# Performance work log

Hardware: AMD Instinct MI355X
Metric: run time of the kernel (lower is better)

The kernel has to match this reference:

```python
import jax, jax.numpy as jnp
import numpy as np
from jax import lax

DN = ('NCHW', 'OIHW', 'NCHW')

def setup_inputs() -> dict:
    key = jax.random.key(0)
    ks = jax.random.split(key, 7)
    s = 0.05  # keep activations tame through 32 chained blocks
    return {
        'x':  jax.random.normal(ks[0], (16, 256, 64, 64), dtype=jnp.float32),
        'w1': jax.random.normal(ks[1], (32, 4, 256, 1, 1), dtype=jnp.float32) * s,
        'b1': jax.random.normal(ks[2], (32, 4), dtype=jnp.float32) * s,
        'w2': jax.random.normal(ks[3], (32, 4, 4, 3, 3), dtype=jnp.float32) * s,
        'b2': jax.random.normal(ks[4], (32, 4), dtype=jnp.float32) * s,
        'w3': jax.random.normal(ks[5], (32, 256, 4, 1, 1), dtype=jnp.float32) * s,
        'b3': jax.random.normal(ks[6], (32, 256), dtype=jnp.float32) * s,
    }

def _block(x, w1, c1, w2, c2, w3, c3):
    # 1x1 reduce -> relu -> 3x3 same -> relu -> 1x1 expand -> relu
    h = jax.nn.relu(lax.conv_general_dilated(x, w1, (1, 1), 'VALID', dimension_numbers=DN)
                    + c1[None, :, None, None])
    h = jax.nn.relu(lax.conv_general_dilated(h, w2, (1, 1), 'SAME', dimension_numbers=DN)
                    + c2[None, :, None, None])
    h = jax.nn.relu(lax.conv_general_dilated(h, w3, (1, 1), 'VALID', dimension_numbers=DN)
                    + c3[None, :, None, None])
    return h

def reference(x, w1, b1, w2, b2, w3, b3):
    def step(carry, ws):
        xc, acc = carry
        xc = _block(xc, *ws)
        return (xc, acc + xc), None
    init = (x, jnp.zeros_like(x))
    (_, acc), _ = lax.scan(step, init, (w1, b1, w2, b2, w3, b3))
    return acc  # sum of all 32 block outputs, [16,256,64,64]
```

## Files before the change

kernel.cpp:

```cpp
#include <hip/hip_runtime.h>


#define NN 16
#define HH 64
#define WW 64
#define CIN 256
#define CB 4
#define NBLK 32
#define PXT 32

__device__ __forceinline__ int pxs(int px) { return px ^ ((px >> 3) & 7); }

__global__ __launch_bounds__(256) void phaseA(
    const float* __restrict__ x, const float* __restrict__ w1,
    const float* __restrict__ b1, float* __restrict__ h1out) {
  __shared__ float4 w1s[CIN];
  __shared__ float4 part[4][WW];
  int tid = threadIdx.x;
  for (int i = tid; i < CIN * CB; i += 256) {
    int o = i >> 8, c = i & 255;
    ((float*)&w1s[c])[o] = w1[i];
  }
  __syncthreads();
  int y = blockIdx.x, n = blockIdx.y;
  int chunk = tid >> 6, px = tid & 63;
  int cbase = chunk * 64;
  const float* xp = x + ((n * CIN + cbase) * HH + y) * WW + px;
  float s0 = 0.f, s1 = 0.f, s2 = 0.f, s3 = 0.f;
#pragma unroll 8
  for (int i = 0; i < 64; ++i) {
    float xv = xp[i * HH * WW];
    float4 wv = w1s[cbase + i];
    s0 = fmaf(xv, wv.x, s0);
    s1 = fmaf(xv, wv.y, s1);
    s2 = fmaf(xv, wv.z, s2);
    s3 = fmaf(xv, wv.w, s3);
  }
  part[chunk][px] = make_float4(s0, s1, s2, s3);
  __syncthreads();
  int px2 = tid >> 2, o = tid & 3;
  float v = ((float*)&part[0][px2])[o] + ((float*)&part[1][px2])[o] +
            ((float*)&part[2][px2])[o] + ((float*)&part[3][px2])[o];
  v += b1[o];
  h1out[((n * HH + y) * WW + px2) * CB + o] = fmaxf(v, 0.f);
}

__global__ __launch_bounds__(256, 2) void phaseB(
    const float* __restrict__ h1in, float* __restrict__ h1out,
    float* __restrict__ h2out,
    const float* __restrict__ w2, const float* __restrict__ b2,
    const float* __restrict__ w3, const float* __restrict__ b3,
    const float* __restrict__ w1n, const float* __restrict__ b1n,
    int compute_next) {
  __shared__ float4 wpk[CIN][2];
  __shared__ float4 b3p[64];
  __shared__ float4 h2sb[128];
  __shared__ __align__(16) float4 uni[2048];
  float4 (*h1t)[18] = (float4(*)[18])uni;
  float4* comb = (float4*)uni;

  int tid = threadIdx.x;
  int tx = blockIdx.x, ty = blockIdx.y, n = blockIdx.z;
  int x0 = tx * 16, y0 = ty * 8;

  {
    int c = tid;
    wpk[c][0] = *(const float4*)&w3[c * 4];
    float4 wt;
    wt.x = w1n[c];
    wt.y = w1n[256 + c];
    wt.z = w1n[512 + c];
    wt.w = w1n[768 + c];
    wpk[c][1] = wt;
    if (tid < 64) b3p[tid] = *(const float4*)&b3[tid * 4];
  }
  if (tid < 180) {
    int cy = tid / 18, cx = tid % 18;
    int gy = y0 + cy - 1, gx = x0 + cx - 1;
    float4 v = make_float4(0.f, 0.f, 0.f, 0.f);
    if (gy >= 0 && gy < HH && gx >= 0 && gx < WW)
      v = *(const float4*)&h1in[((n * HH + gy) * WW + gx) * CB];
    h1t[cy][cx] = v;
  }
  __syncthreads();

  if (tid < 128) {
    int lx = tid & 15, ly = tid >> 4;
    float4 hacc = make_float4(b2[0], b2[1], b2[2], b2[3]);
#pragma unroll
    for (int p = 0; p < 9; ++p) {
      int dy = p / 3, dx = p % 3;
      float4 hv = h1t[ly + dy][lx + dx];
#pragma unroll
      for (int i = 0; i < 4; ++i) {
        float hvi = (i == 0) ? hv.x : (i == 1) ? hv.y : (i == 2) ? hv.z : hv.w;
        hacc.x = fmaf(hvi, w2[(0 * 4 + i) * 9 + p], hacc.x);
        hacc.y = fmaf(hvi, w2[(1 * 4 + i) * 9 + p], hacc.y);
        hacc.z = fmaf(hvi, w2[(2 * 4 + i) * 9 + p], hacc.z);
        hacc.w = fmaf(hvi, w2[(3 * 4 + i) * 9 + p], hacc.w);
      }
    }
    float4 h2 = make_float4(fmaxf(hacc.x, 0.f), fmaxf(hacc.y, 0.f),
                            fmaxf(hacc.z, 0.f), fmaxf(hacc.w, 0.f));
    int gy = y0 + ly, gx = x0 + lx;
    int pxg = (n * HH + gy) * WW + gx;
    *(float4*)&h2out[pxg * CB] = h2;
    h2sb[pxs(tid)] = h2;
  }
  __syncthreads();

  int pg = tid & 15, q = tid >> 4;
  float4 h2r[8];
#pragma unroll
  for (int j = 0; j < 8; ++j) h2r[j] = h2sb[pxs(pg * 8 + j)];

  float4 tp[8];
#pragma unroll
  for (int j = 0; j < 8; ++j) tp[j] = make_float4(0.f, 0.f, 0.f, 0.f);

#pragma unroll
  for (int i4 = 0; i4 < 4; ++i4) {
    float4 bv = b3p[q * 4 + i4];
#pragma unroll
    for (int s = 0; s < 4; ++s) {
      int c = q * 16 + i4 * 4 + s;
      float b = (s == 0) ? bv.x : (s == 1) ? bv.y : (s == 2) ? bv.z : bv.w;
      float4 w3v = wpk[c][0];
      float4 wnv = wpk[c][1];
#pragma unroll
      for (int j = 0; j < 8; ++j) {
        float u = fmaf(h2r[j].x, w3v.x, b);
        u = fmaf(h2r[j].y, w3v.y, u);
        u = fmaf(h2r[j].z, w3v.z, u);
        u = fmaf(h2r[j].w, w3v.w, u);
        float v = fmaxf(u, 0.f);
        tp[j].x = fmaf(v, wnv.x, tp[j].x);
        tp[j].y = fmaf(v, wnv.y, tp[j].y);
        tp[j].z = fmaf(v, wnv.z, tp[j].z);
        tp[j].w = fmaf(v, wnv.w, tp[j].w);
      }
    }
  }

#pragma unroll
  for (int j = 0; j < 8; ++j)
    comb[q * 128 + pxs(pg * 8 + j)] = tp[j];
  __syncthreads();

  if (compute_next && tid < 128) {
    int p = tid;
    float4 t = comb[pxs(p)];
#pragma unroll
    for (int qq = 1; qq < 16; ++qq) {
      float4 pv = comb[qq * 128 + pxs(p)];
      t.x += pv.x; t.y += pv.y; t.z += pv.z; t.w += pv.w;
    }
    float4 r = make_float4(fmaxf(t.x + b1n[0], 0.f), fmaxf(t.y + b1n[1], 0.f),
                           fmaxf(t.z + b1n[2], 0.f), fmaxf(t.w + b1n[3], 0.f));
    int gy = y0 + (p >> 4), gx = x0 + (p & 15);
    *(float4*)&h1out[((n * HH + gy) * WW + gx) * CB] = r;
  }
}

__global__ __launch_bounds__(256, 4) void phaseC(
    const float* __restrict__ h2buf, const float* __restrict__ w3g,
    const float* __restrict__ b3g, float* __restrict__ out) {
  __shared__ float4 h2s[2][PXT];
  __shared__ float tr[CIN][PXT + 1];
  int tid = threadIdx.x;
  int p0 = blockIdx.x * PXT;
  int n = blockIdx.y;
  float acc[PXT];
#pragma unroll
  for (int i = 0; i < PXT; ++i) acc[i] = 0.f;

  if (tid < PXT)
    h2s[0][tid] = *(const float4*)&h2buf[((0 * NN + n) * 4096 + p0 + tid) * 4];
  __syncthreads();

  for (int k = 0; k < NBLK; ++k) {
    float4 wv = *(const float4*)&w3g[(k * 256 + tid) * 4];
    float bv = b3g[k * 256 + tid];
    if (k + 1 < NBLK && tid < PXT)
      h2s[(k + 1) & 1][tid] =
          *(const float4*)&h2buf[(((k + 1) * NN + n) * 4096 + p0 + tid) * 4];
    const float4* hb = h2s[k & 1];
#pragma unroll
    for (int i = 0; i < PXT; ++i) {
      float4 h = hb[i];
      float u = fmaf(h.w, wv.w,
                fmaf(h.z, wv.z, fmaf(h.y, wv.y, fmaf(h.x, wv.x, bv))));
      acc[i] += fmaxf(u, 0.f);
    }
    __syncthreads();
  }

#pragma unroll
  for (int i = 0; i < PXT; ++i) tr[tid][i] = acc[i];
  __syncthreads();
  int xi = tid & 31, cb = tid >> 5;
#pragma unroll
  for (int j = 0; j < 32; ++j) {
    int c = cb + j * 8;
    out[(n * CIN + c) * (HH * WW) + p0 + xi] = tr[c][xi];
  }
}

extern "C" void kernel_launch(void* const* d_in, const int* in_sizes, int n_in,
                              void* d_out, int out_size, void* d_ws, size_t ws_size,
                              hipStream_t stream) {
  const float* x  = (const float*)d_in[0];
  const float* w1 = (const float*)d_in[1];
  const float* b1 = (const float*)d_in[2];
  const float* w2 = (const float*)d_in[3];
  const float* b2 = (const float*)d_in[4];
  const float* w3 = (const float*)d_in[5];
  const float* b3 = (const float*)d_in[6];
  float* out = (float*)d_out;
  float* ws = (float*)d_ws;

  const int STATE = NN * HH * WW * CB;
  float* h1a = ws;
  float* h1b = ws + STATE;
  float* h2  = ws + 2 * STATE;

  phaseA<<<dim3(HH, NN), 256, 0, stream>>>(x, w1, b1, h1a);
  for (int k = 0; k < NBLK; ++k) {
    const float* hin = (k & 1) ? h1b : h1a;
    float* hout = (k & 1) ? h1a : h1b;
    int kn = (k < NBLK - 1) ? k + 1 : NBLK - 1;
    phaseB<<<dim3(4, 8, NN), 256, 0, stream>>>(
        hin, hout, h2 + k * STATE,
        w2 + k * 144, b2 + k * CB, w3 + k * 1024, b3 + k * 256,
        w1 + kn * 1024, b1 + kn * CB, (k < NBLK - 1) ? 1 : 0);
  }
  phaseC<<<dim3((HH * WW) / PXT, NN), 256, 0, stream>>>(h2, w3, b3, out);
}
```

Before: 481.9 us.

## Shrink phaseB tiles to 8x8 and re-tile phaseC over channels and pixels

phaseB now works on 8x8 pixel tiles with twice as many blocks and a launch bound of 4 blocks per CU. Each of its 256 threads computes one output channel of the 3x3 conv, instead of only 128 threads doing all four. The last block returns early and skips the unused next-h1 work. phaseC is re-tiled so each thread owns 4 channels by 8 pixels, prefetches the next block's w3/b3 into registers, and writes its output through a smaller shared transpose in four chunks. The aim is more parallelism and occupancy and fewer redundant loads, at the cost of more halo overhead per tile in phaseB and extra syncs in phaseC's output stage.

Result: no change. 472.9 us (-1.9%).

```diff
diff --git a/kernel.cpp b/kernel.cpp
--- a/kernel.cpp
+++ b/kernel.cpp
@@ -9,7 +9,7 @@
 #define NBLK 32
 #define PXT 32
 
-__device__ __forceinline__ int pxs(int px) { return px ^ ((px >> 3) & 7); }
+__device__ __forceinline__ int swz64(int i) { return i ^ ((i >> 2) & 7); }
 
 __global__ __launch_bounds__(256) void phaseA(
     const float* __restrict__ x, const float* __restrict__ w1,
@@ -45,7 +45,7 @@
   h1out[((n * HH + y) * WW + px2) * CB + o] = fmaxf(v, 0.f);
 }
 
-__global__ __launch_bounds__(256, 2) void phaseB(
+__global__ __launch_bounds__(256, 4) void phaseB(
     const float* __restrict__ h1in, float* __restrict__ h1out,
     float* __restrict__ h2out,
     const float* __restrict__ w2, const float* __restrict__ b2,
@@ -54,14 +54,14 @@
     int compute_next) {
   __shared__ float4 wpk[CIN][2];
   __shared__ float4 b3p[64];
-  __shared__ float4 h2sb[128];
-  __shared__ __align__(16) float4 uni[2048];
-  float4 (*h1t)[18] = (float4(*)[18])uni;
+  __shared__ float4 h2sb[64];
+  __shared__ __align__(16) float4 uni[1024];
+  float4 (*h1t)[12] = (float4(*)[12])uni;
   float4* comb = (float4*)uni;
 
   int tid = threadIdx.x;
-  int tx = blockIdx.x, ty = blockIdx.y, n = blockIdx.z;
-  int x0 = tx * 16, y0 = ty * 8;
+  int x0 = blockIdx.x * 8, y0 = blockIdx.y * 8;
+  int n = blockIdx.z;
 
   {
     int c = tid;
@@ -74,8 +74,8 @@
     wpk[c][1] = wt;
     if (tid < 64) b3p[tid] = *(const float4*)&b3[tid * 4];
   }
-  if (tid < 180) {
-    int cy = tid / 18, cx = tid % 18;
+  if (tid < 100) {
+    int cy = tid / 10, cx = tid % 10;
     int gy = y0 + cy - 1, gx = x0 + cx - 1;
     float4 v = make_float4(0.f, 0.f, 0.f, 0.f);
     if (gy >= 0 && gy < HH && gx >= 0 && gx < WW)
@@ -84,51 +84,48 @@
   }
   __syncthreads();
 
-  if (tid < 128) {
-    int lx = tid & 15, ly = tid >> 4;
-    float4 hacc = make_float4(b2[0], b2[1], b2[2], b2[3]);
+  {
+    int oc = tid & 3, px = tid >> 2;
+    int lx = px & 7, ly = px >> 3;
+    float hacc = b2[oc];
 #pragma unroll
     for (int p = 0; p < 9; ++p) {
       int dy = p / 3, dx = p % 3;
       float4 hv = h1t[ly + dy][lx + dx];
-#pragma unroll
-      for (int i = 0; i < 4; ++i) {
-        float hvi = (i == 0) ? hv.x : (i == 1) ? hv.y : (i == 2) ? hv.z : hv.w;
-        hacc.x = fmaf(hvi, w2[(0 * 4 + i) * 9 + p], hacc.x);
-        hacc.y = fmaf(hvi, w2[(1 * 4 + i) * 9 + p], hacc.y);
-        hacc.z = fmaf(hvi, w2[(2 * 4 + i) * 9 + p], hacc.z);
-        hacc.w = fmaf(hvi, w2[(3 * 4 + i) * 9 + p], hacc.w);
-      }
-    }
-    float4 h2 = make_float4(fmaxf(hacc.x, 0.f), fmaxf(hacc.y, 0.f),
-                            fmaxf(hacc.z, 0.f), fmaxf(hacc.w, 0.f));
+      const float* wr = &w2[oc * 36 + p];
+      hacc = fmaf(hv.x, wr[0], hacc);
+      hacc = fmaf(hv.y, wr[9], hacc);
+      hacc = fmaf(hv.z, wr[18], hacc);
+      hacc = fmaf(hv.w, wr[27], hacc);
+    }
+    float h2v = fmaxf(hacc, 0.f);
     int gy = y0 + ly, gx = x0 + lx;
-    int pxg = (n * HH + gy) * WW + gx;
-    *(float4*)&h2out[pxg * CB] = h2;
-    h2sb[pxs(tid)] = h2;
-  }
-  __syncthreads();
+    h2out[((n * HH + gy) * WW + gx) * CB + oc] = h2v;
+    ((float*)&h2sb[swz64(px)])[oc] = h2v;
+  }
+  __syncthreads();
+  if (!compute_next) return;
 
   int pg = tid & 15, q = tid >> 4;
-  float4 h2r[8];
-#pragma unroll
-  for (int j = 0; j < 8; ++j) h2r[j] = h2sb[pxs(pg * 8 + j)];
-
-  float4 tp[8];
-#pragma unroll
-  for (int j = 0; j < 8; ++j) tp[j] = make_float4(0.f, 0.f, 0.f, 0.f);
+  float4 h2r[4];
+#pragma unroll
+  for (int j = 0; j < 4; ++j) h2r[j] = h2sb[swz64(pg * 4 + j)];
+
+  float4 tp[4];
+#pragma unroll
+  for (int j = 0; j < 4; ++j) tp[j] = make_float4(0.f, 0.f, 0.f, 0.f);
 
 #pragma unroll
   for (int i4 = 0; i4 < 4; ++i4) {
-    float4 bv = b3p[q * 4 + i4];
+    float4 bvv = b3p[q * 4 + i4];
 #pragma unroll
     for (int s = 0; s < 4; ++s) {
       int c = q * 16 + i4 * 4 + s;
-      float b = (s == 0) ? bv.x : (s == 1) ? bv.y : (s == 2) ? bv.z : bv.w;
+      float b = (s == 0) ? bvv.x : (s == 1) ? bvv.y : (s == 2) ? bvv.z : bvv.w;
       float4 w3v = wpk[c][0];
       float4 wnv = wpk[c][1];
 #pragma unroll
-      for (int j = 0; j < 8; ++j) {
+      for (int j = 0; j < 4; ++j) {
         float u = fmaf(h2r[j].x, w3v.x, b);
         u = fmaf(h2r[j].y, w3v.y, u);
         u = fmaf(h2r[j].z, w3v.z, u);
@@ -143,21 +140,21 @@
   }
 
 #pragma unroll
-  for (int j = 0; j < 8; ++j)
-    comb[q * 128 + pxs(pg * 8 + j)] = tp[j];
-  __syncthreads();
-
-  if (compute_next && tid < 128) {
-    int p = tid;
-    float4 t = comb[pxs(p)];
+  for (int j = 0; j < 4; ++j)
+    comb[q * 64 + swz64(pg * 4 + j)] = tp[j];
+  __syncthreads();
+
+  if (tid < 64) {
+    int m = swz64(tid);
+    float4 t = comb[m];
 #pragma unroll
     for (int qq = 1; qq < 16; ++qq) {
-      float4 pv = comb[qq * 128 + pxs(p)];
+      float4 pv = comb[qq * 64 + m];
       t.x += pv.x; t.y += pv.y; t.z += pv.z; t.w += pv.w;
     }
     float4 r = make_float4(fmaxf(t.x + b1n[0], 0.f), fmaxf(t.y + b1n[1], 0.f),
                            fmaxf(t.z + b1n[2], 0.f), fmaxf(t.w + b1n[3], 0.f));
-    int gy = y0 + (p >> 4), gx = x0 + (p & 15);
+    int gy = y0 + (tid >> 3), gx = x0 + (tid & 7);
     *(float4*)&h1out[((n * HH + gy) * WW + gx) * CB] = r;
   }
 }
@@ -166,43 +163,84 @@
     const float* __restrict__ h2buf, const float* __restrict__ w3g,
     const float* __restrict__ b3g, float* __restrict__ out) {
   __shared__ float4 h2s[2][PXT];
-  __shared__ float tr[CIN][PXT + 1];
+  __shared__ float tr[64][PXT + 1];
   int tid = threadIdx.x;
+  int cg = tid & 63;
+  int pg = tid >> 6;
   int p0 = blockIdx.x * PXT;
   int n = blockIdx.y;
-  float acc[PXT];
-#pragma unroll
-  for (int i = 0; i < PXT; ++i) acc[i] = 0.f;
-
+
+  float acc0[8], acc1[8], acc2[8], acc3[8];
+#pragma unroll
+  for (int j = 0; j < 8; ++j) {
+    acc0[j] = 0.f; acc1[j] = 0.f; acc2[j] = 0.f; acc3[j] = 0.f;
+  }
+
+  const float4* wp = (const float4*)&w3g[(cg * 4) * 4];
+  float4 wv0 = wp[0], wv1 = wp[1], wv2 = wp[2], wv3 = wp[3];
+  float4 bv = *(const float4*)&b3g[cg * 4];
   if (tid < PXT)
     h2s[0][tid] = *(const float4*)&h2buf[((0 * NN + n) * 4096 + p0 + tid) * 4];
   __syncthreads();
 
   for (int k = 0; k < NBLK; ++k) {
-    float4 wv = *(const float4*)&w3g[(k * 256 + tid) * 4];
-    float bv = b3g[k * 256 + tid];
-    if (k + 1 < NBLK && tid < PXT)
-      h2s[(k + 1) & 1][tid] =
-          *(const float4*)&h2buf[(((k + 1) * NN + n) * 4096 + p0 + tid) * 4];
-    const float4* hb = h2s[k & 1];
-#pragma unroll
-    for (int i = 0; i < PXT; ++i) {
-      float4 h = hb[i];
-      float u = fmaf(h.w, wv.w,
-                fmaf(h.z, wv.z, fmaf(h.y, wv.y, fmaf(h.x, wv.x, bv))));
-      acc[i] += fmaxf(u, 0.f);
+    float4 nw0, nw1, nw2, nw3, nbv;
+    if (k + 1 < NBLK) {
+      const float4* np = (const float4*)&w3g[((k + 1) * 256 + cg * 4) * 4];
+      nw0 = np[0]; nw1 = np[1]; nw2 = np[2]; nw3 = np[3];
+      nbv = *(const float4*)&b3g[(k + 1) * 256 + cg * 4];
+      if (tid < PXT)
+        h2s[(k + 1) & 1][tid] =
+            *(const float4*)&h2buf[(((k + 1) * NN + n) * 4096 + p0 + tid) * 4];
+    }
+    const float4* hb = &h2s[k & 1][pg * 8];
+#pragma unroll
+    for (int j = 0; j < 8; ++j) {
+      float4 h = hb[j];
+      float u0 = fmaf(h.x, wv0.x, bv.x);
+      u0 = fmaf(h.y, wv0.y, u0); u0 = fmaf(h.z, wv0.z, u0);
+      u0 = fmaf(h.w, wv0.w, u0);
+      acc0[j] += fmaxf(u0, 0.f);
+      float u1 = fmaf(h.x, wv1.x, bv.y);
+      u1 = fmaf(h.y, wv1.y, u1); u1 = fmaf(h.z, wv1.z, u1);
+      u1 = fmaf(h.w, wv1.w, u1);
+      acc1[j] += fmaxf(u1, 0.f);
+      float u2 = fmaf(h.x, wv2.x, bv.z);
+      u2 = fmaf(h.y, wv2.y, u2); u2 = fmaf(h.z, wv2.z, u2);
+      u2 = fmaf(h.w, wv2.w, u2);
+      acc2[j] += fmaxf(u2, 0.f);
+      float u3 = fmaf(h.x, wv3.x, bv.w);
+      u3 = fmaf(h.y, wv3.y, u3); u3 = fmaf(h.z, wv3.z, u3);
+      u3 = fmaf(h.w, wv3.w, u3);
+      acc3[j] += fmaxf(u3, 0.f);
     }
     __syncthreads();
-  }
-
-#pragma unroll
-  for (int i = 0; i < PXT; ++i) tr[tid][i] = acc[i];
-  __syncthreads();
-  int xi = tid & 31, cb = tid >> 5;
-#pragma unroll
-  for (int j = 0; j < 32; ++j) {
-    int c = cb + j * 8;
-    out[(n * CIN + c) * (HH * WW) + p0 + xi] = tr[c][xi];
+    if (k + 1 < NBLK) {
+      wv0 = nw0; wv1 = nw1; wv2 = nw2; wv3 = nw3; bv = nbv;
+    }
+  }
+
+  int xi = tid & 31, cr = tid >> 5;
+#pragma unroll 1
+  for (int ch = 0; ch < 4; ++ch) {
+    if ((cg >> 4) == ch) {
+      int r0 = (cg & 15) * 4;
+      int pb = pg * 8;
+#pragma unroll
+      for (int j = 0; j < 8; ++j) {
+        tr[r0 + 0][pb + j] = acc0[j];
+        tr[r0 + 1][pb + j] = acc1[j];
+        tr[r0 + 2][pb + j] = acc2[j];
+        tr[r0 + 3][pb + j] = acc3[j];
+      }
+    }
+    __syncthreads();
+#pragma unroll
+    for (int j = 0; j < 8; ++j) {
+      int cl = cr * 8 + j;
+      out[(n * CIN + ch * 64 + cl) * (HH * WW) + p0 + xi] = tr[cl][xi];
+    }
+    __syncthreads();
   }
 }
 
@@ -229,7 +267,7 @@
     const float* hin = (k & 1) ? h1b : h1a;
     float* hout = (k & 1) ? h1a : h1b;
     int kn = (k < NBLK - 1) ? k + 1 : NBLK - 1;
-    phaseB<<<dim3(4, 8, NN), 256, 0, stream>>>(
+    phaseB<<<dim3(8, 8, NN), 256, 0, stream>>>(
         hin, hout, h2 + k * STATE,
         w2 + k * 144, b2 + k * CB, w3 + k * 1024, b3 + k * 256,
         w1 + kn * 1024, b1 + kn * CB, (k < NBLK - 1) ? 1 : 0);
```

## Restructure phaseB and phaseC around wave-uniform channel splits with scalar weight loads

Applied to the files above, without the earlier changes.

phaseB now uses 8x8 pixel tiles with one pixel per lane. Each wavefront computes one h2 channel and a quarter of the 256 expand channels, so weights are read at wave-uniform addresses (scalar loads) instead of being staged in shared memory, and the halo window is read straight from global memory. phaseC switches to 64-pixel tiles where each wave owns 64 output channels with uniform weight reads, groups four blocks per prefetch, and writes output through a channel-chunked transpose with float4 stores. The aim is to cut LDS staging, barriers and per-thread weight traffic and to raise occupancy, at the cost of more registers (64 accumulators in phaseC) and redundant halo loads.

Result: slower. 785.3 us (+62.9%).

```diff
diff --git a/kernel.cpp b/kernel.cpp
--- a/kernel.cpp
+++ b/kernel.cpp
@@ -7,9 +7,8 @@
 #define CIN 256
 #define CB 4
 #define NBLK 32
-#define PXT 32
-
-__device__ __forceinline__ int pxs(int px) { return px ^ ((px >> 3) & 7); }
+
+__device__ __forceinline__ int swz64(int i) { return i ^ ((i >> 3) & 7); }
 
 __global__ __launch_bounds__(256) void phaseA(
     const float* __restrict__ x, const float* __restrict__ w1,
@@ -45,119 +44,104 @@
   h1out[((n * HH + y) * WW + px2) * CB + o] = fmaxf(v, 0.f);
 }
 
-__global__ __launch_bounds__(256, 2) void phaseB(
+__global__ __launch_bounds__(256, 4) void phaseB(
     const float* __restrict__ h1in, float* __restrict__ h1out,
     float* __restrict__ h2out,
-    const float* __restrict__ w2, const float* __restrict__ b2,
-    const float* __restrict__ w3, const float* __restrict__ b3,
-    const float* __restrict__ w1n, const float* __restrict__ b1n,
+    const float* __restrict__ w2k,
+    const float* __restrict__ b2k,
+    const float* __restrict__ w3k,
+    const float* __restrict__ b3k,
+    const float* __restrict__ w1n,
+    const float* __restrict__ b1n,
     int compute_next) {
-  __shared__ float4 wpk[CIN][2];
-  __shared__ float4 b3p[64];
-  __shared__ float4 h2sb[128];
-  __shared__ __align__(16) float4 uni[2048];
-  float4 (*h1t)[18] = (float4(*)[18])uni;
-  float4* comb = (float4*)uni;
-
+  __shared__ float h2sb[4][64];
+  __shared__ float4 comb[4][64];
   int tid = threadIdx.x;
-  int tx = blockIdx.x, ty = blockIdx.y, n = blockIdx.z;
-  int x0 = tx * 16, y0 = ty * 8;
-
-  {
-    int c = tid;
-    wpk[c][0] = *(const float4*)&w3[c * 4];
-    float4 wt;
-    wt.x = w1n[c];
-    wt.y = w1n[256 + c];
-    wt.z = w1n[512 + c];
-    wt.w = w1n[768 + c];
-    wpk[c][1] = wt;
-    if (tid < 64) b3p[tid] = *(const float4*)&b3[tid * 4];
-  }
-  if (tid < 180) {
-    int cy = tid / 18, cx = tid % 18;
-    int gy = y0 + cy - 1, gx = x0 + cx - 1;
-    float4 v = make_float4(0.f, 0.f, 0.f, 0.f);
-    if (gy >= 0 && gy < HH && gx >= 0 && gx < WW)
-      v = *(const float4*)&h1in[((n * HH + gy) * WW + gx) * CB];
-    h1t[cy][cx] = v;
-  }
-  __syncthreads();
-
-  if (tid < 128) {
-    int lx = tid & 15, ly = tid >> 4;
-    float4 hacc = make_float4(b2[0], b2[1], b2[2], b2[3]);
-#pragma unroll
-    for (int p = 0; p < 9; ++p) {
-      int dy = p / 3, dx = p % 3;
-      float4 hv = h1t[ly + dy][lx + dx];
-#pragma unroll
-      for (int i = 0; i < 4; ++i) {
-        float hvi = (i == 0) ? hv.x : (i == 1) ? hv.y : (i == 2) ? hv.z : hv.w;
-        hacc.x = fmaf(hvi, w2[(0 * 4 + i) * 9 + p], hacc.x);
-        hacc.y = fmaf(hvi, w2[(1 * 4 + i) * 9 + p], hacc.y);
-        hacc.z = fmaf(hvi, w2[(2 * 4 + i) * 9 + p], hacc.z);
-        hacc.w = fmaf(hvi, w2[(3 * 4 + i) * 9 + p], hacc.w);
+  int lane = tid & 63;
+  int wvu = __builtin_amdgcn_readfirstlane(tid >> 6);
+  int x0 = blockIdx.x * 8, y0 = blockIdx.y * 8, n = blockIdx.z;
+  int lx = lane & 7, ly = lane >> 3;
+  int gy = y0 + ly, gx = x0 + lx;
+
+  float4 win[9];
+  bool interior = (x0 > 0) && (x0 < WW - 8) && (y0 > 0) && (y0 < HH - 8);
+  if (interior) {
+    const float* hp = h1in + ((n * HH + gy - 1) * WW + gx - 1) * CB;
+#pragma unroll
+    for (int dy = 0; dy < 3; ++dy)
+#pragma unroll
+      for (int dx = 0; dx < 3; ++dx)
+        win[dy * 3 + dx] = *(const float4*)(hp + (dy * WW + dx) * CB);
+  } else {
+#pragma unroll
+    for (int dy = 0; dy < 3; ++dy) {
+      int ry = gy - 1 + dy;
+      bool vy = (ry >= 0) && (ry < HH);
+      int ryc = vy ? ry : 0;
+#pragma unroll
+      for (int dx = 0; dx < 3; ++dx) {
+        int rx = gx - 1 + dx;
+        bool vx = (rx >= 0) && (rx < WW);
+        int rxc = vx ? rx : 0;
+        float4 v = *(const float4*)&h1in[((n * HH + ryc) * WW + rxc) * CB];
+        if (!(vy && vx)) v = make_float4(0.f, 0.f, 0.f, 0.f);
+        win[dy * 3 + dx] = v;
       }
     }
-    float4 h2 = make_float4(fmaxf(hacc.x, 0.f), fmaxf(hacc.y, 0.f),
-                            fmaxf(hacc.z, 0.f), fmaxf(hacc.w, 0.f));
-    int gy = y0 + ly, gx = x0 + lx;
-    int pxg = (n * HH + gy) * WW + gx;
-    *(float4*)&h2out[pxg * CB] = h2;
-    h2sb[pxs(tid)] = h2;
-  }
-  __syncthreads();
-
-  int pg = tid & 15, q = tid >> 4;
-  float4 h2r[8];
-#pragma unroll
-  for (int j = 0; j < 8; ++j) h2r[j] = h2sb[pxs(pg * 8 + j)];
-
-  float4 tp[8];
-#pragma unroll
-  for (int j = 0; j < 8; ++j) tp[j] = make_float4(0.f, 0.f, 0.f, 0.f);
-
-#pragma unroll
-  for (int i4 = 0; i4 < 4; ++i4) {
-    float4 bv = b3p[q * 4 + i4];
-#pragma unroll
-    for (int s = 0; s < 4; ++s) {
-      int c = q * 16 + i4 * 4 + s;
-      float b = (s == 0) ? bv.x : (s == 1) ? bv.y : (s == 2) ? bv.z : bv.w;
-      float4 w3v = wpk[c][0];
-      float4 wnv = wpk[c][1];
-#pragma unroll
-      for (int j = 0; j < 8; ++j) {
-        float u = fmaf(h2r[j].x, w3v.x, b);
-        u = fmaf(h2r[j].y, w3v.y, u);
-        u = fmaf(h2r[j].z, w3v.z, u);
-        u = fmaf(h2r[j].w, w3v.w, u);
-        float v = fmaxf(u, 0.f);
-        tp[j].x = fmaf(v, wnv.x, tp[j].x);
-        tp[j].y = fmaf(v, wnv.y, tp[j].y);
-        tp[j].z = fmaf(v, wnv.z, tp[j].z);
-        tp[j].w = fmaf(v, wnv.w, tp[j].w);
-      }
-    }
-  }
-
-#pragma unroll
-  for (int j = 0; j < 8; ++j)
-    comb[q * 128 + pxs(pg * 8 + j)] = tp[j];
-  __syncthreads();
-
-  if (compute_next && tid < 128) {
-    int p = tid;
-    float4 t = comb[pxs(p)];
-#pragma unroll
-    for (int qq = 1; qq < 16; ++qq) {
-      float4 pv = comb[qq * 128 + pxs(p)];
-      t.x += pv.x; t.y += pv.y; t.z += pv.z; t.w += pv.w;
-    }
-    float4 r = make_float4(fmaxf(t.x + b1n[0], 0.f), fmaxf(t.y + b1n[1], 0.f),
-                           fmaxf(t.z + b1n[2], 0.f), fmaxf(t.w + b1n[3], 0.f));
-    int gy = y0 + (p >> 4), gx = x0 + (p & 15);
+  }
+  const float* w2w = w2k + wvu * 36;
+  float hacc = b2k[wvu];
+#pragma unroll
+  for (int p = 0; p < 9; ++p) {
+    hacc = fmaf(win[p].x, w2w[0 + p], hacc);
+    hacc = fmaf(win[p].y, w2w[9 + p], hacc);
+    hacc = fmaf(win[p].z, w2w[18 + p], hacc);
+    hacc = fmaf(win[p].w, w2w[27 + p], hacc);
+  }
+  h2sb[wvu][lane] = fmaxf(hacc, 0.f);
+  __syncthreads();
+
+  float4 h;
+  h.x = h2sb[0][lane];
+  h.y = h2sb[1][lane];
+  h.z = h2sb[2][lane];
+  h.w = h2sb[3][lane];
+  if (tid < 64)
+    *(float4*)&h2out[((n * HH + gy) * WW + gx) * CB] = h;
+
+  if (!compute_next) return;
+
+  float4 tp = make_float4(0.f, 0.f, 0.f, 0.f);
+  const float* w3r = w3k + wvu * 256;
+  const float* b3r = b3k + wvu * 64;
+  const float* w1r0 = w1n + 0 * 256 + wvu * 64;
+  const float* w1r1 = w1n + 1 * 256 + wvu * 64;
+  const float* w1r2 = w1n + 2 * 256 + wvu * 64;
+  const float* w1r3 = w1n + 3 * 256 + wvu * 64;
+#pragma unroll
+  for (int cc = 0; cc < 64; ++cc) {
+    float u = b3r[cc];
+    u = fmaf(h.x, w3r[cc * 4 + 0], u);
+    u = fmaf(h.y, w3r[cc * 4 + 1], u);
+    u = fmaf(h.z, w3r[cc * 4 + 2], u);
+    u = fmaf(h.w, w3r[cc * 4 + 3], u);
+    float v = fmaxf(u, 0.f);
+    tp.x = fmaf(v, w1r0[cc], tp.x);
+    tp.y = fmaf(v, w1r1[cc], tp.y);
+    tp.z = fmaf(v, w1r2[cc], tp.z);
+    tp.w = fmaf(v, w1r3[cc], tp.w);
+  }
+  comb[wvu][swz64(lane)] = tp;
+  __syncthreads();
+
+  if (tid < 64) {
+    int m = swz64(lane);
+    float4 t0 = comb[0][m], t1 = comb[1][m], t2 = comb[2][m], t3 = comb[3][m];
+    float4 r;
+    r.x = fmaxf(t0.x + t1.x + t2.x + t3.x + b1n[0], 0.f);
+    r.y = fmaxf(t0.y + t1.y + t2.y + t3.y + b1n[1], 0.f);
+    r.z = fmaxf(t0.z + t1.z + t2.z + t3.z + b1n[2], 0.f);
+    r.w = fmaxf(t0.w + t1.w + t2.w + t3.w + b1n[3], 0.f);
     *(float4*)&h1out[((n * HH + gy) * WW + gx) * CB] = r;
   }
 }
@@ -165,44 +149,64 @@
 __global__ __launch_bounds__(256, 4) void phaseC(
     const float* __restrict__ h2buf, const float* __restrict__ w3g,
     const float* __restrict__ b3g, float* __restrict__ out) {
-  __shared__ float4 h2s[2][PXT];
-  __shared__ float tr[CIN][PXT + 1];
+  __shared__ float4 h2s[8][64];
+  __shared__ float tr[64][68];
   int tid = threadIdx.x;
-  int p0 = blockIdx.x * PXT;
+  int lane = tid & 63;
+  int wvu = __builtin_amdgcn_readfirstlane(tid >> 6);
+  int p0 = blockIdx.x * 64;
   int n = blockIdx.y;
-  float acc[PXT];
-#pragma unroll
-  for (int i = 0; i < PXT; ++i) acc[i] = 0.f;
-
-  if (tid < PXT)
-    h2s[0][tid] = *(const float4*)&h2buf[((0 * NN + n) * 4096 + p0 + tid) * 4];
-  __syncthreads();
-
-  for (int k = 0; k < NBLK; ++k) {
-    float4 wv = *(const float4*)&w3g[(k * 256 + tid) * 4];
-    float bv = b3g[k * 256 + tid];
-    if (k + 1 < NBLK && tid < PXT)
-      h2s[(k + 1) & 1][tid] =
-          *(const float4*)&h2buf[(((k + 1) * NN + n) * 4096 + p0 + tid) * 4];
-    const float4* hb = h2s[k & 1];
-#pragma unroll
-    for (int i = 0; i < PXT; ++i) {
-      float4 h = hb[i];
-      float u = fmaf(h.w, wv.w,
-                fmaf(h.z, wv.z, fmaf(h.y, wv.y, fmaf(h.x, wv.x, bv))));
-      acc[i] += fmaxf(u, 0.f);
+
+  float acc[64];
+#pragma unroll
+  for (int i = 0; i < 64; ++i) acc[i] = 0.f;
+
+  {
+    int kk = tid >> 6;
+    h2s[kk][swz64(lane)] =
+        *(const float4*)&h2buf[((kk * NN + n) * 4096 + p0 + lane) * 4];
+  }
+  __syncthreads();
+
+  for (int g = 0; g < 8; ++g) {
+    if (g < 7) {
+      int kk = tid >> 6;
+      int k = (g + 1) * 4 + kk;
+      h2s[(((g + 1) & 1) << 2) + kk][swz64(lane)] =
+          *(const float4*)&h2buf[((k * NN + n) * 4096 + p0 + lane) * 4];
+    }
+#pragma unroll
+    for (int kk = 0; kk < 4; ++kk) {
+      int k = g * 4 + kk;
+      float4 h = h2s[((g & 1) << 2) + kk][swz64(lane)];
+      const float* wrow = w3g + (k * 256 + wvu * 64) * 4;
+      const float* brow = b3g + k * 256 + wvu * 64;
+#pragma unroll
+      for (int cc = 0; cc < 64; ++cc) {
+        float u = brow[cc];
+        u = fmaf(h.x, wrow[cc * 4 + 0], u);
+        u = fmaf(h.y, wrow[cc * 4 + 1], u);
+        u = fmaf(h.z, wrow[cc * 4 + 2], u);
+        u = fmaf(h.w, wrow[cc * 4 + 3], u);
+        acc[cc] += fmaxf(u, 0.f);
+      }
     }
     __syncthreads();
   }
 
-#pragma unroll
-  for (int i = 0; i < PXT; ++i) tr[tid][i] = acc[i];
-  __syncthreads();
-  int xi = tid & 31, cb = tid >> 5;
-#pragma unroll
-  for (int j = 0; j < 32; ++j) {
-    int c = cb + j * 8;
-    out[(n * CIN + c) * (HH * WW) + p0 + xi] = tr[c][xi];
+  int r = tid >> 2, c4 = (tid & 3) * 16;
+  for (int ch = 0; ch < 4; ++ch) {
+    if (wvu == ch) {
+#pragma unroll
+      for (int cc = 0; cc < 64; ++cc) tr[cc][lane] = acc[cc];
+    }
+    __syncthreads();
+#pragma unroll
+    for (int j = 0; j < 4; ++j) {
+      float4 v = *(const float4*)&tr[r][c4 + j * 4];
+      *(float4*)&out[(n * CIN + ch * 64 + r) * (HH * WW) + p0 + c4 + j * 4] = v;
+    }
+    __syncthreads();
   }
 }
 
@@ -229,10 +233,10 @@
     const float* hin = (k & 1) ? h1b : h1a;
     float* hout = (k & 1) ? h1a : h1b;
     int kn = (k < NBLK - 1) ? k + 1 : NBLK - 1;
-    phaseB<<<dim3(4, 8, NN), 256, 0, stream>>>(
+    phaseB<<<dim3(8, 8, NN), 256, 0, stream>>>(
         hin, hout, h2 + k * STATE,
         w2 + k * 144, b2 + k * CB, w3 + k * 1024, b3 + k * 256,
         w1 + kn * 1024, b1 + kn * CB, (k < NBLK - 1) ? 1 : 0);
   }
-  phaseC<<<dim3((HH * WW) / PXT, NN), 256, 0, stream>>>(h2, w3, b3, out);
-}
+  phaseC<<<dim3((HH * WW) / 64, NN), 256, 0, stream>>>(h2, w3, b3, out);
+}
```
